# Optimization experiments

Hardware: AMD Instinct MI355X
Metric: run time of the kernel (lower is better)

Reference implementation:

```python
import jax, jax.numpy as jnp
import numpy as np

TOPK = 3
IOU_THRESHOLD = 0.5


def setup_inputs() -> dict:
    key = jax.random.key(0)
    k0, k1, k2, k3 = jax.random.split(key, 4)
    S, N, TGT_PER_VID = 256, 128, 4
    M = S * TGT_PER_VID          # 1024 target moments total
    P = N * N                    # 16384 valid proposals (mask2d all ones)
    start_offset = jax.random.normal(k0, (S, P), dtype=jnp.float32) * 0.1
    end_offset = jax.random.normal(k1, (S, P), dtype=jnp.float32) * 0.1
    # target moments: (start, end) in [0,1], start <= end
    tgt_moments = jnp.sort(jax.random.uniform(k2, (M, 2), dtype=jnp.float32), axis=1)
    num_targets = jnp.full((S,), TGT_PER_VID, dtype=jnp.int32)  # sums to M
    iou2ds = jax.random.uniform(k3, (M, N, N), dtype=jnp.float32)
    mask2d = jnp.ones((N, N), dtype=bool)
    return {
        "start_offset": start_offset,
        "end_offset": end_offset,
        "tgt_moments": tgt_moments,
        "num_targets": num_targets,
        "iou2ds": iou2ds,
        "mask2d": mask2d,
    }


def reference(start_offset, end_offset, tgt_moments, num_targets, iou2ds, mask2d):
    M, N, _ = iou2ds.shape
    S, P = start_offset.shape
    # map each of the M targets back to its source video (repeat_interleave)
    scatter_m2s = jnp.repeat(jnp.arange(S), num_targets, total_repeat_length=M)
    so = start_offset[scatter_m2s]  # [M, P]
    eo = end_offset[scatter_m2s]    # [M, P]
    # row-major nonzero positions of mask2d (== torch masked_select ordering)
    rows, cols = jnp.nonzero(mask2d, size=P)
    iou1ds = iou2ds[:, rows, cols]  # [M, P]
    # top-k scatter mask + IoU-threshold mask
    _, topk_idx = jax.lax.top_k(iou1ds, TOPK)  # [M, TOPK]
    target_mask = jnp.zeros((M, P), dtype=start_offset.dtype)
    target_mask = target_mask.at[jnp.arange(M)[:, None], topk_idx].set(1.0)
    target_mask = jnp.where(iou1ds > IOU_THRESHOLD, 1.0, target_mask)
    # scores2ds_to_moments: proposal (row, col) -> moment (row/N, (col+1)/N)
    starts = rows.astype(start_offset.dtype) / N                 # [P]
    ends = (cols.astype(start_offset.dtype) + 1.0) / N           # [P]
    start_offset_target = tgt_moments[:, 0:1] - starts[None, :]  # [M, P]
    end_offset_target = tgt_moments[:, 1:2] - ends[None, :]      # [M, P]
    loss = jnp.abs(so - start_offset_target) + jnp.abs(eo - end_offset_target)
    return (loss * target_mask).sum() / target_mask.sum()
```

## Files before the change

### kernel.cpp

```cpp
#include <hip/hip_runtime.h>
#include <math.h>

#define TOPK_N 3
#define IOU_THR 0.5f
#define NCNT 8
#define THREADS 512
#define NW (THREADS / 64)
#define SENT 0x7fffffff

__device__ __forceinline__ bool better(float va, int ia, float vb, int ib) {
    return (va > vb) || (va == vb && ia < ib);
}

__device__ __forceinline__ void merge3(float& a0, float& a1, float& a2,
                                       int& x0, int& x1, int& x2,
                                       float b0, float b1, float b2,
                                       int y0, int y1, int y2) {
    bool t0 = better(a0, x0, b0, y0);
    float ov0 = t0 ? a0 : b0;  int oi0 = t0 ? x0 : y0;
    float ahv = t0 ? a1 : a0;  int ahi = t0 ? x1 : x0;
    float a2v = t0 ? a2 : a1;  int a2i = t0 ? x2 : x1;
    float bhv = t0 ? b0 : b1;  int bhi = t0 ? y0 : y1;
    float b2v = t0 ? b1 : b2;  int b2i = t0 ? y1 : y2;
    bool t1 = better(ahv, ahi, bhv, bhi);
    float ov1 = t1 ? ahv : bhv; int oi1 = t1 ? ahi : bhi;
    float cav = t1 ? a2v : ahv; int cai = t1 ? a2i : ahi;
    float cbv = t1 ? bhv : b2v; int cbi = t1 ? bhi : b2i;
    bool t2 = better(cav, cai, cbv, cbi);
    a0 = ov0; a1 = ov1; a2 = t2 ? cav : cbv;
    x0 = oi0; x1 = oi1; x2 = t2 ? cai : cbi;
}

__global__ void prep_kernel(const int* __restrict__ num_targets,
                            const int* __restrict__ mask2d,
                            int* __restrict__ scatter,
                            int* __restrict__ counts,
                            int S, int M, int P) {
    const int bid = blockIdx.x;
    const int tid = threadIdx.x;

    if (bid < NCNT) {
        const int P4 = P >> 2;
        const int4* __restrict__ m4 = (const int4*)mask2d;
        int c = 0;
        for (int q = bid * 256 + tid; q < P4; q += NCNT * 256) {
            const int4 v = m4[q];
            c += (v.x != 0) + (v.y != 0) + (v.z != 0) + (v.w != 0);
        }
        if (bid == 0) {
            for (int j = (P4 << 2) + tid; j < P; j += 256)
                c += (mask2d[j] != 0);
        }
        __shared__ int red[256];
        red[tid] = c;
        __syncthreads();
        for (int st = 128; st > 0; st >>= 1) {
            if (tid < st) red[tid] += red[tid + st];
            __syncthreads();
        }
        if (tid == 0) counts[bid] = red[0];
    } else {
        __shared__ int cum[1025];
        __shared__ int scn[256];
        const int chunk = (S + 255) / 256;
        const int sbase = tid * chunk;
        int local[4];
        int csum = 0;
        for (int k = 0; k < chunk && k < 4; ++k) {
            int s = sbase + k;
            int v = (s < S) ? num_targets[s] : 0;
            csum += v;
            local[k] = csum;
        }
        scn[tid] = csum;
        __syncthreads();
        for (int d = 1; d < 256; d <<= 1) {
            int v = scn[tid];
            int add = (tid >= d) ? scn[tid - d] : 0;
            __syncthreads();
            scn[tid] = v + add;
            __syncthreads();
        }
        {
            int excl = scn[tid] - csum;
            for (int k = 0; k < chunk && k < 4; ++k) {
                int s = sbase + k;
                if (s < S) cum[s + 1] = excl + local[k];
            }
            if (tid == 0) cum[0] = 0;
        }
        __syncthreads();
        const int total = cum[S];
        for (int m = tid; m < M; m += 256) {
            int mm = m;
            if (mm >= total) mm = (total > 0) ? (total - 1) : 0;
            int lo = 0, hi = S - 1;
            while (lo < hi) {
                int mid = (lo + hi) >> 1;
                if (cum[mid + 1] <= mm) lo = mid + 1; else hi = mid;
            }
            scatter[m] = lo;
        }
    }
}

__global__ void build_kernel(const int* __restrict__ counts,
                             const int* __restrict__ mask2d,
                             int* __restrict__ rcidx,
                             float* __restrict__ starts,
                             float* __restrict__ ends,
                             int* __restrict__ flag,
                             int N, int P) {
    const int tid = threadIdx.x;
    __shared__ int scan[256];

    scan[tid] = (tid < NCNT) ? counts[tid] : 0;
    __syncthreads();
    for (int st = 128; st > 0; st >>= 1) {
        if (tid < st) scan[tid] += scan[tid + st];
        __syncthreads();
    }
    const int K_all = scan[0];
    const int f = (K_all == P && (P & 3) == 0 && (N & (N - 1)) == 0 && N >= 4) ? 1 : 0;
    if (tid == 0) flag[0] = f;
    if (f) return;
    __syncthreads();

    const int per = (P + 255) / 256;
    const int base = tid * per;
    int cnt = 0;
    for (int k = 0; k < per; ++k) {
        int j = base + k;
        if (j < P && mask2d[j] != 0) cnt++;
    }
    scan[tid] = cnt;
    __syncthreads();
    for (int d = 1; d < 256; d <<= 1) {
        int v = scan[tid];
        int add = (tid >= d) ? scan[tid - d] : 0;
        __syncthreads();
        scan[tid] = v + add;
        __syncthreads();
    }
    const int K = scan[255];
    int pos = scan[tid] - cnt;

    const float fN = (float)N;
    for (int k = 0; k < per; ++k) {
        int j = base + k;
        if (j < P && mask2d[j] != 0) {
            int r = j / N;
            int c = j - r * N;
            rcidx[pos]  = j;
            starts[pos] = (float)r / fN;
            ends[pos]   = (float)(c + 1) / fN;
            pos++;
        }
    }
    __syncthreads();
    for (int j = K + tid; j < P; j += 256) {
        rcidx[j]  = 0;
        starts[j] = 0.0f;
        ends[j]   = 1.0f / fN;
    }
}

__global__ __launch_bounds__(THREADS, 8)
void loss_kernel(const float* __restrict__ start_offset,
                 const float* __restrict__ end_offset,
                 const float* __restrict__ tgt_moments,
                 const int* __restrict__ scatter,
                 const float* __restrict__ iou2ds,
                 const int* __restrict__ rcidx,
                 const float* __restrict__ starts,
                 const float* __restrict__ ends,
                 double* __restrict__ psum,
                 int* __restrict__ pcnt,
                 const int* __restrict__ flag,
                 int P, int M, int N) {
    const int bid = blockIdx.x;
    const int m = ((M & 7) == 0) ? ((bid & 7) * (M >> 3) + (bid >> 3)) : bid;
    const int tid = threadIdx.x;
    const int s   = scatter[m];
    const int fp  = flag[0];

    const float* __restrict__ so_row  = start_offset + (size_t)s * P;
    const float* __restrict__ eo_row  = end_offset   + (size_t)s * P;
    const float* __restrict__ iou_row = iou2ds       + (size_t)m * P;
    const float tgt0 = tgt_moments[2 * m];
    const float tgt1 = tgt_moments[2 * m + 1];

    const int   lgN  = 31 - __clz(N);
    const float invN = 1.0f / (float)N;

    float lsum = 0.0f;
    int   lcnt = 0;

    float v0 = -INFINITY, v1 = -INFINITY, v2 = -INFINITY;
    int   i0 = SENT, i1 = SENT, i2 = SENT;

#define PROC(v, jj, so_, eo_, A_, B_)                                       \
    do {                                                                    \
        const bool b0 = (v) > v0;                                           \
        const bool b1 = (v) > v1;                                           \
        const bool b2 = (v) > v2;                                           \
        v2 = b1 ? v1 : (b2 ? (v) : v2);  i2 = b1 ? i1 : (b2 ? (jj) : i2);   \
        v1 = b0 ? v0 : (b1 ? (v) : v1);  i1 = b0 ? i0 : (b1 ? (jj) : i1);   \
        v0 = b0 ? (v) : v0;              i0 = b0 ? (jj) : i0;               \
        const bool sel = (v) > IOU_THR;                                     \
        const float l_ = fabsf((so_) - (A_)) + fabsf((eo_) - (B_));         \
        lsum += sel ? l_ : 0.0f;                                            \
        lcnt += sel ? 1 : 0;                                                \
    } while (0)

#define PROC4(vi, vs, ve, q)                                                \
    do {                                                                    \
        const int j_  = (q) << 2;                                           \
        const int r_  = j_ >> lgN;                                          \
        const int c_  = j_ & (N - 1);                                       \
        const float A_  = tgt0 - (float)r_ * invN;      \
        const float en0 = (float)(c_ + 1) * invN;     \
        PROC((vi).x, j_ + 0, (vs).x, (ve).x, A_, tgt1 - en0);               \
        PROC((vi).y, j_ + 1, (vs).y, (ve).y, A_, tgt1 - (en0 + invN));      \
        PROC((vi).z, j_ + 2, (vs).z, (ve).z, A_, tgt1 - (en0 + 2.0f*invN)); \
        PROC((vi).w, j_ + 3, (vs).w, (ve).w, A_, tgt1 - (en0 + 3.0f*invN)); \
    } while (0)

    if (fp && (P & (8 * THREADS - 1)) == 0) {
        const float4* __restrict__ iou4 = (const float4*)iou_row;
        const float4* __restrict__ so4  = (const float4*)so_row;
        const float4* __restrict__ eo4  = (const float4*)eo_row;
        const int ITERS = P >> (2 + 1 + 9);
        int qA = tid;
        for (int it = 0; it < ITERS; ++it) {
            const int qB = qA + THREADS;
            const float4 iA = iou4[qA]; const float4 iB = iou4[qB];
            const float4 sA = so4[qA];  const float4 sB = so4[qB];
            const float4 eA = eo4[qA];  const float4 eB = eo4[qB];
            PROC4(iA, sA, eA, qA);
            PROC4(iB, sB, eB, qB);
            qA += 2 * THREADS;
        }
    } else if (fp) {
        const float4* __restrict__ iou4 = (const float4*)iou_row;
        const float4* __restrict__ so4  = (const float4*)so_row;
        const float4* __restrict__ eo4  = (const float4*)eo_row;
        const int P4 = P >> 2;
        for (int q = tid; q < P4; q += THREADS) {
            const float4 vi = iou4[q];
            const float4 vs = so4[q];
            const float4 ve = eo4[q];
            PROC4(vi, vs, ve, q);
        }
    } else {
        for (int j = tid; j < P; j += THREADS) {
            const int   idx = rcidx[j];
            const float v   = iou_row[idx];
            const float A_  = tgt0 - starts[j];
            const float B_  = tgt1 - ends[j];
            PROC(v, j, so_row[j], eo_row[j], A_, B_);
        }
    }
#undef PROC4
#undef PROC

    for (int d = 1; d < 64; d <<= 1) {
        float bv0 = __shfl_xor(v0, d), bv1 = __shfl_xor(v1, d), bv2 = __shfl_xor(v2, d);
        int   by0 = __shfl_xor(i0, d), by1 = __shfl_xor(i1, d), by2 = __shfl_xor(i2, d);
        merge3(v0, v1, v2, i0, i1, i2, bv0, bv1, bv2, by0, by1, by2);
    }
    double dsum = (double)lsum;
    for (int d = 1; d < 64; d <<= 1) dsum += __shfl_xor(dsum, d);
    for (int d = 1; d < 64; d <<= 1) lcnt += __shfl_xor(lcnt, d);

    __shared__ float  wv[NW][3];
    __shared__ int    wi[NW][3];
    __shared__ double wsum[NW];
    __shared__ int    wcnt[NW];
    const int wid  = tid >> 6;
    const int lane = tid & 63;
    if (lane == 0) {
        wv[wid][0] = v0; wv[wid][1] = v1; wv[wid][2] = v2;
        wi[wid][0] = i0; wi[wid][1] = i1; wi[wid][2] = i2;
        wsum[wid] = dsum; wcnt[wid] = lcnt;
    }
    __syncthreads();

    if (tid == 0) {
        float a0 = wv[0][0], a1 = wv[0][1], a2 = wv[0][2];
        int   x0 = wi[0][0], x1 = wi[0][1], x2 = wi[0][2];
        double S = wsum[0];
        int    C = wcnt[0];
        for (int w = 1; w < NW; ++w) {
            merge3(a0, a1, a2, x0, x1, x2,
                   wv[w][0], wv[w][1], wv[w][2],
                   wi[w][0], wi[w][1], wi[w][2]);
            S += wsum[w];
            C += wcnt[w];
        }
#define ADDTOP(vk, jk)                                                      \
        do {                                                                \
            if ((jk) != SENT && !((vk) > IOU_THR)) {                        \
                float st_, en_;                                             \
                if (fp) {                                                   \
                    int r_ = (jk) >> lgN, c_ = (jk) & (N - 1);              \
                    st_ = (float)r_ * invN; en_ = (float)(c_ + 1) * invN;   \
                } else { st_ = starts[jk]; en_ = ends[jk]; }                \
                S += (double)(fabsf(so_row[jk] - (tgt0 - st_)) +            \
                              fabsf(eo_row[jk] - (tgt1 - en_)));            \
                C += 1;                                                     \
            }                                                               \
        } while (0)
        ADDTOP(a0, x0);
        ADDTOP(a1, x1);
        ADDTOP(a2, x2);
#undef ADDTOP
        psum[bid] = S;
        pcnt[bid] = C;
    }
}

__global__ void finalize_kernel(const double* __restrict__ psum,
                                const int* __restrict__ pcnt,
                                int M, float* __restrict__ out) {
    __shared__ double sd[256];
    __shared__ int    sc[256];
    const int tid = threadIdx.x;
    double a = 0.0;
    int    c = 0;
    for (int i = tid; i < M; i += 256) { a += psum[i]; c += pcnt[i]; }
    sd[tid] = a; sc[tid] = c;
    __syncthreads();
    for (int str = 128; str > 0; str >>= 1) {
        if (tid < str) { sd[tid] += sd[tid + str]; sc[tid] += sc[tid + str]; }
        __syncthreads();
    }
    if (tid == 0) out[0] = (float)(sd[0] / (double)sc[0]);
}

extern "C" void kernel_launch(void* const* d_in, const int* in_sizes, int n_in,
                              void* d_out, int out_size, void* d_ws, size_t ws_size,
                              hipStream_t stream) {
    const float* start_offset = (const float*)d_in[0];
    const float* end_offset   = (const float*)d_in[1];
    const float* tgt_moments  = (const float*)d_in[2];
    const int*   num_targets  = (const int*)d_in[3];
    const float* iou2ds       = (const float*)d_in[4];
    const int*   mask2d       = (const int*)d_in[5];

    const int S = in_sizes[3];
    const int M = in_sizes[2] / 2;
    const int P = in_sizes[0] / S;
    const int NN = in_sizes[5];
    int N = 1;
    while ((long long)N * N < (long long)NN) N++;

    char* ws = (char*)d_ws;
    size_t off = 0;
    int*    flag    = (int*)(ws + off);    off += 16;
    int*    counts  = (int*)(ws + off);    off += (NCNT * 4 + 15) & ~(size_t)15;
    int*    scatter = (int*)(ws + off);    off += ((size_t)M * 4 + 15) & ~(size_t)15;
    int*    rcidx   = (int*)(ws + off);    off += ((size_t)P * 4 + 15) & ~(size_t)15;
    float*  starts  = (float*)(ws + off);  off += ((size_t)P * 4 + 15) & ~(size_t)15;
    float*  ends    = (float*)(ws + off);  off += ((size_t)P * 4 + 15) & ~(size_t)15;
    double* psum    = (double*)(ws + off); off += ((size_t)M * 8 + 15) & ~(size_t)15;
    int*    pcnt    = (int*)(ws + off);    off += ((size_t)M * 4 + 15) & ~(size_t)15;

    prep_kernel<<<NCNT + 1, 256, 0, stream>>>(num_targets, mask2d, scatter, counts,
                                              S, M, P);
    build_kernel<<<1, 256, 0, stream>>>(counts, mask2d, rcidx, starts, ends, flag, N, P);
    loss_kernel<<<M, THREADS, 0, stream>>>(start_offset, end_offset, tgt_moments,
                                           scatter, iou2ds, rcidx, starts, ends,
                                           psum, pcnt, flag, P, M, N);
    finalize_kernel<<<1, 256, 0, stream>>>(psum, pcnt, M, (float*)d_out);
}
```

Baseline: 34.55 us.

## Merge prep and build into one init kernel, use nontemporal IoU loads and med3 top-k

Combines the two setup kernels into a single 1024-thread block kernel, removing one launch and the counts round-trip through global memory. The IoU rows are loaded with nontemporal loads because they are read only once, which should leave more cache room for the reused start/end offset rows. The top-3 value update is rewritten with fmax/fmed3 instead of select chains. Risks: the mask count now runs in one block rather than eight, and the non-participating threads must match the scan's barrier count exactly.

```diff
diff --git a/kernel.cpp b/kernel.cpp
--- a/kernel.cpp
+++ b/kernel.cpp
@@ -1,12 +1,12 @@
 #include <hip/hip_runtime.h>
 #include <math.h>
 
-#define TOPK_N 3
 #define IOU_THR 0.5f
-#define NCNT 8
 #define THREADS 512
 #define NW (THREADS / 64)
 #define SENT 0x7fffffff
+
+typedef float fx4 __attribute__((ext_vector_type(4)));
 
 __device__ __forceinline__ bool better(float va, int ia, float vb, int ib) {
     return (va > vb) || (va == vb && ia < ib);
@@ -31,37 +31,47 @@
     x0 = oi0; x1 = oi1; x2 = t2 ? cai : cbi;
 }
 
-__global__ void prep_kernel(const int* __restrict__ num_targets,
-                            const int* __restrict__ mask2d,
-                            int* __restrict__ scatter,
-                            int* __restrict__ counts,
-                            int S, int M, int P) {
-    const int bid = blockIdx.x;
+__device__ __forceinline__ float4 ntload4(const float4* p) {
+    fx4 v = __builtin_nontemporal_load((const fx4*)p);
+    return make_float4(v.x, v.y, v.z, v.w);
+}
+
+__global__ __launch_bounds__(1024)
+void init_kernel(const int* __restrict__ num_targets,
+                 const int* __restrict__ mask2d,
+                 int* __restrict__ scatter,
+                 int* __restrict__ rcidx,
+                 float* __restrict__ starts,
+                 float* __restrict__ ends,
+                 int* __restrict__ flag,
+                 int S, int M, int N, int P) {
     const int tid = threadIdx.x;
-
-    if (bid < NCNT) {
+    __shared__ int red[1024];
+    __shared__ int cum[1025];
+    __shared__ int scn[256];
+
+    {
         const int P4 = P >> 2;
         const int4* __restrict__ m4 = (const int4*)mask2d;
         int c = 0;
-        for (int q = bid * 256 + tid; q < P4; q += NCNT * 256) {
+        for (int q = tid; q < P4; q += 1024) {
             const int4 v = m4[q];
             c += (v.x != 0) + (v.y != 0) + (v.z != 0) + (v.w != 0);
         }
-        if (bid == 0) {
-            for (int j = (P4 << 2) + tid; j < P; j += 256)
-                c += (mask2d[j] != 0);
-        }
-        __shared__ int red[256];
+        for (int j = (P4 << 2) + tid; j < P; j += 1024)
+            c += (mask2d[j] != 0);
         red[tid] = c;
-        __syncthreads();
-        for (int st = 128; st > 0; st >>= 1) {
-            if (tid < st) red[tid] += red[tid + st];
-            __syncthreads();
-        }
-        if (tid == 0) counts[bid] = red[0];
-    } else {
-        __shared__ int cum[1025];
-        __shared__ int scn[256];
+    }
+    __syncthreads();
+    for (int st = 512; st > 0; st >>= 1) {
+        if (tid < st) red[tid] += red[tid + st];
+        __syncthreads();
+    }
+    const int K_all = red[0];
+    const int f = (K_all == P && (P & 3) == 0 && (N & (N - 1)) == 0 && N >= 4) ? 1 : 0;
+    if (tid == 0) flag[0] = f;
+
+    if (tid < 256) {
         const int chunk = (S + 255) / 256;
         const int sbase = tid * chunk;
         int local[4];
@@ -81,87 +91,68 @@
             scn[tid] = v + add;
             __syncthreads();
         }
-        {
-            int excl = scn[tid] - csum;
-            for (int k = 0; k < chunk && k < 4; ++k) {
-                int s = sbase + k;
-                if (s < S) cum[s + 1] = excl + local[k];
+        int excl = scn[tid] - csum;
+        for (int k = 0; k < chunk && k < 4; ++k) {
+            int s = sbase + k;
+            if (s < S) cum[s + 1] = excl + local[k];
+        }
+        if (tid == 0) cum[0] = 0;
+    } else {
+        __syncthreads();
+        for (int d = 1; d < 256; d <<= 1) { __syncthreads(); __syncthreads(); }
+    }
+    __syncthreads();
+    const int total = cum[S];
+    for (int m = tid; m < M; m += 1024) {
+        int mm = m;
+        if (mm >= total) mm = (total > 0) ? (total - 1) : 0;
+        int lo = 0, hi = S - 1;
+        while (lo < hi) {
+            int mid = (lo + hi) >> 1;
+            if (cum[mid + 1] <= mm) lo = mid + 1; else hi = mid;
+        }
+        scatter[m] = lo;
+    }
+    if (f) return;
+    __syncthreads();
+
+    if (tid < 256) {
+        const int per = (P + 255) / 256;
+        const int base = tid * per;
+        int cnt = 0;
+        for (int k = 0; k < per; ++k) {
+            int j = base + k;
+            if (j < P && mask2d[j] != 0) cnt++;
+        }
+        scn[tid] = cnt;
+        __syncthreads();
+        for (int d = 1; d < 256; d <<= 1) {
+            int v = scn[tid];
+            int add = (tid >= d) ? scn[tid - d] : 0;
+            __syncthreads();
+            scn[tid] = v + add;
+            __syncthreads();
+        }
+        const int K = scn[255];
+        int pos = scn[tid] - cnt;
+        const float fN = (float)N;
+        for (int k = 0; k < per; ++k) {
+            int j = base + k;
+            if (j < P && mask2d[j] != 0) {
+                int r = j / N;
+                int c = j - r * N;
+                rcidx[pos]  = j;
+                starts[pos] = (float)r / fN;
+                ends[pos]   = (float)(c + 1) / fN;
+                pos++;
             }
-            if (tid == 0) cum[0] = 0;
-        }
-        __syncthreads();
-        const int total = cum[S];
-        for (int m = tid; m < M; m += 256) {
-            int mm = m;
-            if (mm >= total) mm = (total > 0) ? (total - 1) : 0;
-            int lo = 0, hi = S - 1;
-            while (lo < hi) {
-                int mid = (lo + hi) >> 1;
-                if (cum[mid + 1] <= mm) lo = mid + 1; else hi = mid;
-            }
-            scatter[m] = lo;
-        }
-    }
-}
-
-__global__ void build_kernel(const int* __restrict__ counts,
-                             const int* __restrict__ mask2d,
-                             int* __restrict__ rcidx,
-                             float* __restrict__ starts,
-                             float* __restrict__ ends,
-                             int* __restrict__ flag,
-                             int N, int P) {
-    const int tid = threadIdx.x;
-    __shared__ int scan[256];
-
-    scan[tid] = (tid < NCNT) ? counts[tid] : 0;
-    __syncthreads();
-    for (int st = 128; st > 0; st >>= 1) {
-        if (tid < st) scan[tid] += scan[tid + st];
-        __syncthreads();
-    }
-    const int K_all = scan[0];
-    const int f = (K_all == P && (P & 3) == 0 && (N & (N - 1)) == 0 && N >= 4) ? 1 : 0;
-    if (tid == 0) flag[0] = f;
-    if (f) return;
-    __syncthreads();
-
-    const int per = (P + 255) / 256;
-    const int base = tid * per;
-    int cnt = 0;
-    for (int k = 0; k < per; ++k) {
-        int j = base + k;
-        if (j < P && mask2d[j] != 0) cnt++;
-    }
-    scan[tid] = cnt;
-    __syncthreads();
-    for (int d = 1; d < 256; d <<= 1) {
-        int v = scan[tid];
-        int add = (tid >= d) ? scan[tid - d] : 0;
-        __syncthreads();
-        scan[tid] = v + add;
-        __syncthreads();
-    }
-    const int K = scan[255];
-    int pos = scan[tid] - cnt;
-
-    const float fN = (float)N;
-    for (int k = 0; k < per; ++k) {
-        int j = base + k;
-        if (j < P && mask2d[j] != 0) {
-            int r = j / N;
-            int c = j - r * N;
-            rcidx[pos]  = j;
-            starts[pos] = (float)r / fN;
-            ends[pos]   = (float)(c + 1) / fN;
-            pos++;
-        }
-    }
-    __syncthreads();
-    for (int j = K + tid; j < P; j += 256) {
-        rcidx[j]  = 0;
-        starts[j] = 0.0f;
-        ends[j]   = 1.0f / fN;
+        }
+        __syncthreads();
+        for (int j = K + tid; j < P; j += 256) {
+            rcidx[j]  = 0;
+            starts[j] = 0.0f;
+            ends[j]   = 1.0f / fN;
+        }
     }
 }
 
@@ -181,8 +172,8 @@
     const int bid = blockIdx.x;
     const int m = ((M & 7) == 0) ? ((bid & 7) * (M >> 3) + (bid >> 3)) : bid;
     const int tid = threadIdx.x;
+    const int fp  = flag[0];
     const int s   = scatter[m];
-    const int fp  = flag[0];
 
     const float* __restrict__ so_row  = start_offset + (size_t)s * P;
     const float* __restrict__ eo_row  = end_offset   + (size_t)s * P;
@@ -204,9 +195,13 @@
         const bool b0 = (v) > v0;                                           \
         const bool b1 = (v) > v1;                                           \
         const bool b2 = (v) > v2;                                           \
-        v2 = b1 ? v1 : (b2 ? (v) : v2);  i2 = b1 ? i1 : (b2 ? (jj) : i2);   \
-        v1 = b0 ? v0 : (b1 ? (v) : v1);  i1 = b0 ? i0 : (b1 ? (jj) : i1);   \
-        v0 = b0 ? (v) : v0;              i0 = b0 ? (jj) : i0;               \
+        const float nv0 = fmaxf(v0, (v));                                   \
+        const float nv1 = __builtin_amdgcn_fmed3f((v), v0, v1);             \
+        const float nv2 = __builtin_amdgcn_fmed3f((v), v1, v2);             \
+        i2 = b1 ? i1 : (b2 ? (jj) : i2);                                    \
+        i1 = b0 ? i0 : (b1 ? (jj) : i1);                                    \
+        i0 = b0 ? (jj) : i0;                                                \
+        v0 = nv0; v1 = nv1; v2 = nv2;                                       \
         const bool sel = (v) > IOU_THR;                                     \
         const float l_ = fabsf((so_) - (A_)) + fabsf((eo_) - (B_));         \
         lsum += sel ? l_ : 0.0f;                                            \
@@ -230,11 +225,11 @@
         const float4* __restrict__ iou4 = (const float4*)iou_row;
         const float4* __restrict__ so4  = (const float4*)so_row;
         const float4* __restrict__ eo4  = (const float4*)eo_row;
-        const int ITERS = P >> (2 + 1 + 9);
+        const int ITERS = P / (8 * THREADS);
         int qA = tid;
         for (int it = 0; it < ITERS; ++it) {
             const int qB = qA + THREADS;
-            const float4 iA = iou4[qA]; const float4 iB = iou4[qB];
+            const float4 iA = ntload4(iou4 + qA); const float4 iB = ntload4(iou4 + qB);
             const float4 sA = so4[qA];  const float4 sB = so4[qB];
             const float4 eA = eo4[qA];  const float4 eB = eo4[qB];
             PROC4(iA, sA, eA, qA);
@@ -247,7 +242,7 @@
         const float4* __restrict__ eo4  = (const float4*)eo_row;
         const int P4 = P >> 2;
         for (int q = tid; q < P4; q += THREADS) {
-            const float4 vi = iou4[q];
+            const float4 vi = ntload4(iou4 + q);
             const float4 vs = so4[q];
             const float4 ve = eo4[q];
             PROC4(vi, vs, ve, q);
@@ -358,7 +353,6 @@
     char* ws = (char*)d_ws;
     size_t off = 0;
     int*    flag    = (int*)(ws + off);    off += 16;
-    int*    counts  = (int*)(ws + off);    off += (NCNT * 4 + 15) & ~(size_t)15;
     int*    scatter = (int*)(ws + off);    off += ((size_t)M * 4 + 15) & ~(size_t)15;
     int*    rcidx   = (int*)(ws + off);    off += ((size_t)P * 4 + 15) & ~(size_t)15;
     float*  starts  = (float*)(ws + off);  off += ((size_t)P * 4 + 15) & ~(size_t)15;
@@ -366,9 +360,8 @@
     double* psum    = (double*)(ws + off); off += ((size_t)M * 8 + 15) & ~(size_t)15;
     int*    pcnt    = (int*)(ws + off);    off += ((size_t)M * 4 + 15) & ~(size_t)15;
 
-    prep_kernel<<<NCNT + 1, 256, 0, stream>>>(num_targets, mask2d, scatter, counts,
-                                              S, M, P);
-    build_kernel<<<1, 256, 0, stream>>>(counts, mask2d, rcidx, starts, ends, flag, N, P);
+    init_kernel<<<1, 1024, 0, stream>>>(num_targets, mask2d, scatter, rcidx,
+                                        starts, ends, flag, S, M, N, P);
     loss_kernel<<<M, THREADS, 0, stream>>>(start_offset, end_offset, tgt_moments,
                                            scatter, iou2ds, rcidx, starts, ends,
                                            psum, pcnt, flag, P, M, N);
```

Measured after the change: 34.57 us. No clear change (+0.1%).
